# Performance work log

Measured on AMD Instinct MI355X. Metric: run time of the kernel, lower is better.

The kernel has to match this reference:

```python
import jax, jax.numpy as jnp
import numpy as np

D_MODEL = 2048
N_HEAD = 16
HEAD_DIM = D_MODEL // N_HEAD
FFN_DIM = 4 * D_MODEL
B, T = 2, 2048
EPS = float(np.finfo(np.float32).eps)  # torch nn.RMSNorm default eps


def _rmsnorm(x, w):
    return x * jax.lax.rsqrt(jnp.mean(x * x, axis=-1, keepdims=True) + EPS) * w


def _apply_rope(x, cos, sin):
    # x: (B,H,T,hd); cos/sin: (T,hd) with each frequency repeated twice
    cos_pair = cos[..., 0::2]
    sin_pair = sin[..., 0::2]
    x_even = x[..., 0::2]
    x_odd = x[..., 1::2]
    rot_even = x_even * cos_pair - x_odd * sin_pair
    rot_odd = x_odd * cos_pair + x_even * sin_pair
    # interleave back: (..., hd//2, 2) -> (..., hd)
    return jnp.stack([rot_even, rot_odd], axis=-1).reshape(x.shape)


def setup_inputs() -> dict:
    key = jax.random.key(0)
    ks = jax.random.split(key, 9)
    x = jax.random.normal(ks[0], (B, T, D_MODEL), dtype=jnp.float32)
    # real RoPE cache: freqs repeated twice along last axis (interleaved-pair)
    inv_freq = 1.0 / (10000.0 ** (np.arange(0, HEAD_DIM, 2, dtype=np.float32) / HEAD_DIM))
    ang = np.arange(T, dtype=np.float32)[:, None] * inv_freq[None, :]  # (T, hd/2)
    ang2 = np.repeat(ang, 2, axis=-1)  # (T, hd)
    rope_cache = jnp.stack([jnp.cos(jnp.asarray(ang2)), jnp.sin(jnp.asarray(ang2))], axis=0)
    s = 0.02
    return {
        "x": x,
        "rope_cache": rope_cache,
        "attn_norm_w": jnp.ones((D_MODEL,), jnp.float32),
        "qkv_w": s * jax.random.normal(ks[1], (3 * D_MODEL, D_MODEL), jnp.float32),
        "q_norm_w": jnp.ones((HEAD_DIM,), jnp.float32),
        "k_norm_w": jnp.ones((HEAD_DIM,), jnp.float32),
        "out_proj_w": s * jax.random.normal(ks[2], (D_MODEL, D_MODEL), jnp.float32),
        "mlp_norm_w": jnp.ones((D_MODEL,), jnp.float32),
        "mlp_in_w": s * jax.random.normal(ks[3], (FFN_DIM, D_MODEL), jnp.float32),
        "mlp_out_w": s * jax.random.normal(ks[4], (D_MODEL, FFN_DIM), jnp.float32),
    }


def reference(x, rope_cache, attn_norm_w, qkv_w, q_norm_w, k_norm_w,
              out_proj_w, mlp_norm_w, mlp_in_w, mlp_out_w):
    cos, sin = rope_cache[0], rope_cache[1]
    b, t, d = x.shape
    h = _rmsnorm(x, attn_norm_w)
    qkv = h @ qkv_w.T  # (B,T,3D)
    q, k, v = jnp.split(qkv, 3, axis=-1)
    q = q.reshape(b, t, N_HEAD, HEAD_DIM).transpose(0, 2, 1, 3)
    k = k.reshape(b, t, N_HEAD, HEAD_DIM).transpose(0, 2, 1, 3)
    v = v.reshape(b, t, N_HEAD, HEAD_DIM).transpose(0, 2, 1, 3)
    q = _rmsnorm(_apply_rope(q, cos, sin), q_norm_w)
    k = _rmsnorm(_apply_rope(k, cos, sin), k_norm_w)
    scale = 1.0 / jnp.sqrt(jnp.float32(HEAD_DIM))
    scores = jnp.einsum('bhqd,bhkd->bhqk', q, k) * scale
    causal = jnp.tril(jnp.ones((t, t), dtype=bool))
    scores = jnp.where(causal, scores, -jnp.inf)
    attn = jax.nn.softmax(scores, axis=-1)
    attn_out = jnp.einsum('bhqk,bhkd->bhqd', attn, v)
    attn_out = attn_out.transpose(0, 2, 1, 3).reshape(b, t, d)
    x = x + attn_out @ out_proj_w.T
    m = _rmsnorm(x, mlp_norm_w) @ mlp_in_w.T
    m = jnp.square(jax.nn.relu(m))
    return x + m @ mlp_out_w.T
```

## Files before the change

### kernel.cpp

```cpp
#include <hip/hip_runtime.h>
#include <stdint.h>

#define TT 2048
#define DM 2048
#define NH 16
#define HD 128
#define FFN 8192
#define MR 4096
#define EPSF 1.1920928955078125e-07f
#define NEGBIG (-1.0e30f)

typedef __attribute__((ext_vector_type(8))) short short8;
typedef __attribute__((ext_vector_type(4))) float f32x4;
typedef unsigned short u16;
typedef unsigned int u32;

__device__ __forceinline__ float bf2f(u32 u) {
    return __uint_as_float((u & 0xffffu) << 16);
}
__device__ __forceinline__ u16 f2bf(float f) {
    u32 x = __float_as_uint(f);
    return (u16)((x + 0x7fffu + ((x >> 16) & 1u)) >> 16);
}
__device__ __forceinline__ void load8f(const u16* p, float* v) {
    uint4 d = *(const uint4*)p;
    v[0] = bf2f(d.x); v[1] = bf2f(d.x >> 16);
    v[2] = bf2f(d.y); v[3] = bf2f(d.y >> 16);
    v[4] = bf2f(d.z); v[5] = bf2f(d.z >> 16);
    v[6] = bf2f(d.w); v[7] = bf2f(d.w >> 16);
}
__device__ __forceinline__ void load8f32(const float* p, float* v) {
    float4 a = *(const float4*)p, b = *(const float4*)(p + 4);
    v[0]=a.x; v[1]=a.y; v[2]=a.z; v[3]=a.w; v[4]=b.x; v[5]=b.y; v[6]=b.z; v[7]=b.w;
}
__device__ __forceinline__ void store8bf(u16* p, const float* v) {
    uint4 o;
    o.x = (u32)f2bf(v[0]) | ((u32)f2bf(v[1]) << 16);
    o.y = (u32)f2bf(v[2]) | ((u32)f2bf(v[3]) << 16);
    o.z = (u32)f2bf(v[4]) | ((u32)f2bf(v[5]) << 16);
    o.w = (u32)f2bf(v[6]) | ((u32)f2bf(v[7]) << 16);
    *(uint4*)p = o;
}
__device__ __forceinline__ uint4 cvt8_f32_bf16(const float* p) {
    float4 a = *(const float4*)p, b = *(const float4*)(p + 4);
    uint4 o;
    o.x = (u32)f2bf(a.x) | ((u32)f2bf(a.y) << 16);
    o.y = (u32)f2bf(a.z) | ((u32)f2bf(a.w) << 16);
    o.z = (u32)f2bf(b.x) | ((u32)f2bf(b.y) << 16);
    o.w = (u32)f2bf(b.z) | ((u32)f2bf(b.w) << 16);
    return o;
}
__device__ __forceinline__ void gload_lds16(const void* g, void* l) {
    __builtin_amdgcn_global_load_lds((const __attribute__((address_space(1))) u32*)g,
                                     (__attribute__((address_space(3))) u32*)l, 16, 0, 0);
}

__global__ __launch_bounds__(256)
void cvt_w(const float* __restrict__ S, u16* __restrict__ D) {
    size_t i = ((size_t)blockIdx.x * 256 + threadIdx.x) * 8;
    *(uint4*)(D + i) = cvt8_f32_bf16(S + i);
}

__global__ __launch_bounds__(256)
void rmsnorm_k(const float* __restrict__ X, const float* __restrict__ W, u16* __restrict__ O) {
    const int row = blockIdx.x, tid = threadIdx.x;
    float v[8];
    load8f32(X + (size_t)row * DM + tid * 8, v);
    float ssq = 0.f;
#pragma unroll
    for (int i = 0; i < 8; ++i) ssq += v[i] * v[i];
#pragma unroll
    for (int d = 1; d < 64; d <<= 1) ssq += __shfl_xor(ssq, d);
    __shared__ float red[4];
    if ((tid & 63) == 0) red[tid >> 6] = ssq;
    __syncthreads();
    ssq = red[0] + red[1] + red[2] + red[3];
    const float inv = rsqrtf(ssq * (1.f / DM) + EPSF);
    float wv[8], o[8];
    load8f32(W + tid * 8, wv);
#pragma unroll
    for (int i = 0; i < 8; ++i) o[i] = v[i] * inv * wv[i];
    store8bf(O + (size_t)row * DM + tid * 8, o);
}

template<int EPI>
__global__ __launch_bounds__(256)
void gemm_bt(const u16* __restrict__ A, const u16* __restrict__ Bw,
             const float* __restrict__ Res, void* __restrict__ Cp,
             int M, int N, int K, int ldb) {
    __shared__ alignas(16) u16 As[128 * 32];
    __shared__ alignas(16) u16 Bs[128 * 32];
    const int tid = threadIdx.x;
    const int lane = tid & 63, w = tid >> 6;
    const int quad = lane >> 4, col = lane & 15;
    const int n0 = blockIdx.x * 128, m0 = blockIdx.y * 128;
    const int wm = (w >> 1) * 64, wn = (w & 1) * 64;

    const int c0 = tid, c1 = tid + 256;
    const int ar0 = c0 >> 2, aq0 = (c0 & 3) ^ ((ar0 >> 1) & 3);
    const int ar1 = c1 >> 2, aq1 = (c1 & 3) ^ ((ar1 >> 1) & 3);
    const u16* agp0 = A  + (size_t)(m0 + ar0) * K + aq0 * 8;
    const u16* agp1 = A  + (size_t)(m0 + ar1) * K + aq1 * 8;
    const u16* bgp0 = Bw + (size_t)(n0 + ar0) * ldb + aq0 * 8;
    const u16* bgp1 = Bw + (size_t)(n0 + ar1) * ldb + aq1 * 8;
    u16* al0 = As + c0 * 8; u16* al1 = As + c1 * 8;
    u16* bl0 = Bs + c0 * 8; u16* bl1 = Bs + c1 * 8;

    int aoff[4], boff[4];
#pragma unroll
    for (int i = 0; i < 4; ++i) {
        int r = wm + i * 16 + col;
        aoff[i] = r * 32 + (quad ^ ((r >> 1) & 3)) * 8;
        r = wn + i * 16 + col;
        boff[i] = r * 32 + (quad ^ ((r >> 1) & 3)) * 8;
    }

    f32x4 acc[4][4];
#pragma unroll
    for (int i = 0; i < 4; ++i)
#pragma unroll
        for (int j = 0; j < 4; ++j) acc[i][j] = (f32x4){0.f, 0.f, 0.f, 0.f};

    for (int kt = 0; kt < K; kt += 32) {
        __syncthreads();
        gload_lds16(agp0 + kt, al0);
        gload_lds16(agp1 + kt, al1);
        gload_lds16(bgp0 + kt, bl0);
        gload_lds16(bgp1 + kt, bl1);
        __syncthreads();
        short8 af[4], bfr[4];
#pragma unroll
        for (int i = 0; i < 4; ++i) af[i] = *(const short8*)(As + aoff[i]);
#pragma unroll
        for (int i = 0; i < 4; ++i) bfr[i] = *(const short8*)(Bs + boff[i]);
#pragma unroll
        for (int mi = 0; mi < 4; ++mi)
#pragma unroll
            for (int ni = 0; ni < 4; ++ni)
                acc[mi][ni] = __builtin_amdgcn_mfma_f32_16x16x32_bf16(af[mi], bfr[ni], acc[mi][ni], 0, 0, 0);
    }

#pragma unroll
    for (int mi = 0; mi < 4; ++mi)
#pragma unroll
        for (int ni = 0; ni < 4; ++ni) {
            const int rbase = m0 + wm + mi * 16 + quad * 4;
            const int cc = n0 + wn + ni * 16 + col;
#pragma unroll
            for (int rr = 0; rr < 4; ++rr) {
                float v = acc[mi][ni][rr];
                size_t idx = (size_t)(rbase + rr) * N + cc;
                if (EPI == 0) ((u16*)Cp)[idx] = f2bf(v);
                else if (EPI == 1) { float t = fmaxf(v, 0.f); ((u16*)Cp)[idx] = f2bf(t * t); }
                else ((float*)Cp)[idx] = v + Res[idx];
            }
        }
}

__global__ __launch_bounds__(256)
void rope_split_k(const u16* __restrict__ QKV, const float* __restrict__ RC,
                  const float* __restrict__ QW, const float* __restrict__ KW,
                  u16* __restrict__ Qo, u16* __restrict__ Ko, u16* __restrict__ Vo) {
    const int row = blockIdx.x;
    const int t = row & (TT - 1), b = row >> 11;
    const int tid = threadIdx.x, h = tid >> 4, j = tid & 15;
    const size_t qb = (size_t)row * (3 * DM) + h * HD + j * 8;
    float q[8], k[8], cs[8], sn[8];
    load8f(QKV + qb, q);
    load8f(QKV + qb + DM, k);
    uint4 vv = *(const uint4*)(QKV + qb + 2 * DM);
    load8f32(RC + (size_t)t * HD + j * 8, cs);
    load8f32(RC + (size_t)(TT + t) * HD + j * 8, sn);
    float qr[8], kr[8];
#pragma unroll
    for (int p = 0; p < 4; ++p) {
        float c = cs[2 * p], s = sn[2 * p];
        qr[2*p]   = q[2*p]   * c - q[2*p+1] * s;
        qr[2*p+1] = q[2*p+1] * c + q[2*p]   * s;
        kr[2*p]   = k[2*p]   * c - k[2*p+1] * s;
        kr[2*p+1] = k[2*p+1] * c + k[2*p]   * s;
    }
    float sq = 0.f, sk = 0.f;
#pragma unroll
    for (int i = 0; i < 8; ++i) { sq += qr[i] * qr[i]; sk += kr[i] * kr[i]; }
#pragma unroll
    for (int d = 1; d < 16; d <<= 1) { sq += __shfl_xor(sq, d); sk += __shfl_xor(sk, d); }
    const float iq = rsqrtf(sq * (1.f / HD) + EPSF);
    const float ik = rsqrtf(sk * (1.f / HD) + EPSF);
    float qw[8], kw[8], oq[8], ok[8];
    load8f32(QW + j * 8, qw); load8f32(KW + j * 8, kw);
#pragma unroll
    for (int i = 0; i < 8; ++i) { oq[i] = qr[i] * iq * qw[i]; ok[i] = kr[i] * ik * kw[i]; }
    const size_t ob = ((size_t)(b * NH + h) * TT + t) * HD + j * 8;
    store8bf(Qo + ob, oq);
    store8bf(Ko + ob, ok);
    *(uint4*)(Vo + ob) = vv;
}

__global__ __launch_bounds__(256)
void transpose_v(const u16* __restrict__ V, u16* __restrict__ Vt) {
    __shared__ alignas(16) u16 tile[64][72];
    const int bh = blockIdx.z;
    const int t0 = blockIdx.x * 64, d0 = blockIdx.y * 64;
    const int tid = threadIdx.x;
#pragma unroll
    for (int i = 0; i < 2; ++i) {
        int c = i * 256 + tid;
        int r = c >> 3, cc = (c & 7) * 8;
        *(uint4*)(&tile[r][cc]) = *(const uint4*)(V + ((size_t)bh * TT + t0 + r) * HD + d0 + cc);
    }
    __syncthreads();
#pragma unroll
    for (int i = 0; i < 2; ++i) {
        int c = i * 256 + tid;
        int dc = c >> 3, rr = (c & 7) * 8;
        u16 tmp[8];
#pragma unroll
        for (int kk = 0; kk < 8; ++kk) tmp[kk] = tile[rr + kk][dc];
        uint4 o;
        o.x = (u32)tmp[0] | ((u32)tmp[1] << 16);
        o.y = (u32)tmp[2] | ((u32)tmp[3] << 16);
        o.z = (u32)tmp[4] | ((u32)tmp[5] << 16);
        o.w = (u32)tmp[6] | ((u32)tmp[7] << 16);
        *(uint4*)(Vt + ((size_t)bh * HD + d0 + dc) * TT + t0 + rr) = o;
    }
}

__global__ __launch_bounds__(256)
void attn_k(const u16* __restrict__ Q, const u16* __restrict__ Kg,
            const u16* __restrict__ Vt, u16* __restrict__ O) {
    __shared__ alignas(16) u16 k_lds[2][64 * 128];
    __shared__ alignas(16) u16 v_lds[2][128 * 64];
    __shared__ alignas(16) u16 p_lds[4 * 16 * 72];
    const int qt = gridDim.x - 1 - blockIdx.x;
    const int bh = blockIdx.y;
    const int tid = threadIdx.x, lane = tid & 63, w = tid >> 6;
    const int quad = lane >> 4, col = lane & 15;
    const int qbase = qt * 64;
    const int qrow = qbase + w * 16 + col;

    short8 qf[4];
    const u16* qp = Q + ((size_t)bh * TT + qrow) * HD;
#pragma unroll
    for (int s = 0; s < 4; ++s) qf[s] = *(const short8*)(qp + s * 32 + quad * 8);

    const u16* kp[4]; const u16* vp[4];
#pragma unroll
    for (int i = 0; i < 4; ++i) {
        int lin = i * 256 + tid;
        int r = lin >> 4, sl = lin & 15;
        int gq = sl ^ (r & 15);
        kp[i] = Kg + ((size_t)bh * TT + r) * HD + gq * 8;
    }
#pragma unroll
    for (int i = 0; i < 4; ++i) {
        int lin = i * 256 + tid;
        int r = lin >> 3, sl = lin & 7;
        int gq = sl ^ (r & 7);
        vp[i] = Vt + ((size_t)bh * HD + r) * TT + gq * 8;
    }

    f32x4 oacc[8];
#pragma unroll
    for (int i = 0; i < 8; ++i) oacc[i] = (f32x4){0.f, 0.f, 0.f, 0.f};
    float mrow[4] = {NEGBIG, NEGBIG, NEGBIG, NEGBIG};
    float lrow[4] = {0.f, 0.f, 0.f, 0.f};
    const float scale = 0.08838834764831845f;

    u16* kcur = k_lds[0]; u16* knxt = k_lds[1];
    u16* vcur = v_lds[0]; u16* vnxt = v_lds[1];
#pragma unroll
    for (int i = 0; i < 4; ++i) gload_lds16(kp[i], kcur + (i * 256 + tid) * 8);
#pragma unroll
    for (int i = 0; i < 4; ++i) gload_lds16(vp[i], vcur + (i * 256 + tid) * 8);

    for (int kt = 0; kt <= qt; ++kt) {
        const int kb = kt * 64;
        __syncthreads();

        if (kt < qt) {
            const int kb2 = kb + 64;
#pragma unroll
            for (int i = 0; i < 4; ++i) gload_lds16(kp[i] + (size_t)kb2 * HD, knxt + (i * 256 + tid) * 8);
#pragma unroll
            for (int i = 0; i < 4; ++i) gload_lds16(vp[i] + kb2, vnxt + (i * 256 + tid) * 8);
        }

        f32x4 sfr[4];
#pragma unroll
        for (int ni = 0; ni < 4; ++ni) sfr[ni] = (f32x4){0.f, 0.f, 0.f, 0.f};
        __builtin_amdgcn_s_setprio(1);
#pragma unroll
        for (int ni = 0; ni < 4; ++ni) {
            const int r = ni * 16 + col;
#pragma unroll
            for (int s = 0; s < 4; ++s) {
                int sl = (s * 4 + quad) ^ (r & 15);
                short8 kf = *(const short8*)(kcur + r * 128 + sl * 8);
                sfr[ni] = __builtin_amdgcn_mfma_f32_16x16x32_bf16(qf[s], kf, sfr[ni], 0, 0, 0);
            }
        }
        __builtin_amdgcn_s_setprio(0);
        const bool diag = (kt == qt);
#pragma unroll
        for (int ni = 0; ni < 4; ++ni) {
            const int key = kb + ni * 16 + col;
#pragma unroll
            for (int rr = 0; rr < 4; ++rr) {
                float v = sfr[ni][rr] * scale;
                int qv = qbase + w * 16 + quad * 4 + rr;
                if (diag && key > qv) v = NEGBIG;
                sfr[ni][rr] = v;
            }
        }
        float mx[4];
#pragma unroll
        for (int rr = 0; rr < 4; ++rr)
            mx[rr] = fmaxf(fmaxf(sfr[0][rr], sfr[1][rr]), fmaxf(sfr[2][rr], sfr[3][rr]));
#pragma unroll
        for (int d = 1; d < 16; d <<= 1)
#pragma unroll
            for (int rr = 0; rr < 4; ++rr) mx[rr] = fmaxf(mx[rr], __shfl_xor(mx[rr], d));
        if (__any((mx[0] > mrow[0]) || (mx[1] > mrow[1]) ||
                  (mx[2] > mrow[2]) || (mx[3] > mrow[3]))) {
#pragma unroll
            for (int rr = 0; rr < 4; ++rr) {
                float mn = fmaxf(mrow[rr], mx[rr]);
                float a = __expf(mrow[rr] - mn);
                mrow[rr] = mn;
                lrow[rr] *= a;
#pragma unroll
                for (int i = 0; i < 8; ++i) oacc[i][rr] *= a;
            }
        }
        float rs[4] = {0.f, 0.f, 0.f, 0.f};
#pragma unroll
        for (int ni = 0; ni < 4; ++ni)
#pragma unroll
            for (int rr = 0; rr < 4; ++rr) {
                float p = __expf(sfr[ni][rr] - mrow[rr]);
                sfr[ni][rr] = p;
                rs[rr] += p;
            }
#pragma unroll
        for (int d = 1; d < 16; d <<= 1)
#pragma unroll
            for (int rr = 0; rr < 4; ++rr) rs[rr] += __shfl_xor(rs[rr], d);
#pragma unroll
        for (int rr = 0; rr < 4; ++rr) lrow[rr] += rs[rr];
#pragma unroll
        for (int ni = 0; ni < 4; ++ni)
#pragma unroll
            for (int rr = 0; rr < 4; ++rr)
                p_lds[(w * 16 + quad * 4 + rr) * 72 + ni * 16 + col] = f2bf(sfr[ni][rr]);
        __builtin_amdgcn_s_setprio(1);
#pragma unroll
        for (int ks = 0; ks < 2; ++ks) {
            short8 pa = *(const short8*)(p_lds + (w * 16 + col) * 72 + ks * 32 + quad * 8);
#pragma unroll
            for (int di = 0; di < 8; ++di) {
                int r = di * 16 + col;
                int sl = (ks * 4 + quad) ^ (r & 7);
                short8 vb = *(const short8*)(vcur + r * 64 + sl * 8);
                oacc[di] = __builtin_amdgcn_mfma_f32_16x16x32_bf16(pa, vb, oacc[di], 0, 0, 0);
            }
        }
        __builtin_amdgcn_s_setprio(0);
        { u16* t = kcur; kcur = knxt; knxt = t; }
        { u16* t = vcur; vcur = vnxt; vnxt = t; }
    }
    const int b = bh >> 4, h = bh & 15;
#pragma unroll
    for (int di = 0; di < 8; ++di)
#pragma unroll
        for (int rr = 0; rr < 4; ++rr) {
            int trow = qbase + w * 16 + quad * 4 + rr;
            float ov = oacc[di][rr] / lrow[rr];
            O[((size_t)(b * TT + trow)) * DM + h * HD + di * 16 + col] = f2bf(ov);
        }
}

extern "C" void kernel_launch(void* const* d_in, const int* in_sizes, int n_in,
                              void* d_out, int out_size, void* d_ws, size_t ws_size,
                              hipStream_t stream) {
    const float* x    = (const float*)d_in[0];
    const float* rc   = (const float*)d_in[1];
    const float* anw  = (const float*)d_in[2];
    const float* qkvw = (const float*)d_in[3];
    const float* qnw  = (const float*)d_in[4];
    const float* knw  = (const float*)d_in[5];
    const float* opw  = (const float*)d_in[6];
    const float* mnw  = (const float*)d_in[7];
    const float* miw  = (const float*)d_in[8];
    const float* mow  = (const float*)d_in[9];

    char* ws = (char*)d_ws;
    u16* hbuf = (u16*)(ws);
    u16* Wq   = (u16*)(ws + (16ll  << 20));
    u16* Wmi  = (u16*)(ws + (16ll  << 20));
    u16* vt   = (u16*)(ws + (16ll  << 20));
    u16* aout = (u16*)(ws + (32ll  << 20));
    u16* Wmo  = (u16*)(ws + (48ll  << 20));
    u16* qkv  = (u16*)(ws + (48ll  << 20));
    u16* mbuf = (u16*)(ws + (80ll  << 20));
    u16* qh   = (u16*)(ws + (96ll  << 20));
    u16* Wo   = (u16*)(ws + (112ll << 20));
    u16* kh   = (u16*)(ws + (112ll << 20));
    u16* vh   = (u16*)(ws);
    float* xo = (float*)d_out;

    rmsnorm_k<<<MR, 256, 0, stream>>>(x, anw, hbuf);
    cvt_w<<<6144, 256, 0, stream>>>(qkvw, Wq);
    gemm_bt<0><<<dim3(48, 32), 256, 0, stream>>>(hbuf, Wq, nullptr, qkv, MR, 3 * DM, DM, DM);
    rope_split_k<<<MR, 256, 0, stream>>>(qkv, rc, qnw, knw, qh, kh, vh);
    transpose_v<<<dim3(32, 2, 32), 256, 0, stream>>>(vh, vt);
    attn_k<<<dim3(32, 32), 256, 0, stream>>>(qh, kh, vt, aout);
    cvt_w<<<2048, 256, 0, stream>>>(opw, Wo);
    cvt_w<<<8192, 256, 0, stream>>>(mow, Wmo);
    gemm_bt<2><<<dim3(16, 32), 256, 0, stream>>>(aout, Wo, x, xo, MR, DM, DM, DM);
    rmsnorm_k<<<MR, 256, 0, stream>>>(xo, mnw, hbuf);
    cvt_w<<<8192, 256, 0, stream>>>(miw, Wmi);
    gemm_bt<1><<<dim3(32, 32), 256, 0, stream>>>(hbuf, Wmi, nullptr, mbuf, MR, FFN / 2, DM, DM);
    gemm_bt<2><<<dim3(16, 32), 256, 0, stream>>>(mbuf, Wmo, xo, xo, MR, DM, FFN / 2, FFN);
    gemm_bt<1><<<dim3(32, 32), 256, 0, stream>>>(hbuf, Wmi + (size_t)(FFN / 2) * DM, nullptr, mbuf, MR, FFN / 2, DM, DM);
    gemm_bt<2><<<dim3(16, 32), 256, 0, stream>>>(mbuf, Wmo + FFN / 2, xo, xo, MR, DM, FFN / 2, FFN);
}
```

Before: 1.061 ms.

## Add 256x256-tile 4-stage pipelined GEMM for QKV and MLP-in projections

Introduces a new GEMM kernel with 256x256 output tiles, 512 threads, a 4-deep LDS ring buffer fed by direct global-to-LDS loads, XOR-swizzled LDS layout, and an XCD-aware block index remap. It replaces the smaller-tile GEMM for the QKV projection and both MLP-in halves, aiming to raise arithmetic intensity per loaded byte and hide memory latency. The larger tile uses 128 KB of LDS and many accumulator registers, which limits occupancy and yields fewer blocks (256-384) for the 256 compute units.

```diff
diff --git a/kernel.cpp b/kernel.cpp
--- a/kernel.cpp
+++ b/kernel.cpp
@@ -153,6 +153,105 @@
                 if (EPI == 0) ((u16*)Cp)[idx] = f2bf(v);
                 else if (EPI == 1) { float t = fmaxf(v, 0.f); ((u16*)Cp)[idx] = f2bf(t * t); }
                 else ((float*)Cp)[idx] = v + Res[idx];
+            }
+        }
+}
+
+template<int EPI>
+__global__ __launch_bounds__(512, 2)
+void gemm_big(const u16* __restrict__ A, const u16* __restrict__ Bw,
+              void* __restrict__ Cp, int M, int N, int K, int ldb) {
+    __shared__ alignas(16) u16 As[4][256 * 32];
+    __shared__ alignas(16) u16 Bs[4][256 * 32];
+    const int tid = threadIdx.x;
+    const int lane = tid & 63, w = tid >> 6;
+    const int wr = w >> 2, wc = w & 3;
+    const int quad = lane >> 4, colL = lane & 15;
+
+    const int nbx = N >> 8;
+    const int nwg = gridDim.x;
+    const int cpx = nwg >> 3;
+    const int bid = blockIdx.x;
+    const int swz = (bid & 7) * cpx + (bid >> 3);
+    const int by = swz / nbx, bx = swz - by * nbx;
+    const int m0 = by << 8, n0 = bx << 8;
+
+    const int r0 = tid >> 2,       q0 = (tid & 3) ^ ((r0 >> 1) & 3);
+    const int p1 = tid + 512;
+    const int r1 = p1 >> 2,        q1 = (p1 & 3) ^ ((r1 >> 1) & 3);
+    const u16* agp0 = A  + (size_t)(m0 + r0) * K   + q0 * 8;
+    const u16* agp1 = A  + (size_t)(m0 + r1) * K   + q1 * 8;
+    const u16* bgp0 = Bw + (size_t)(n0 + r0) * ldb + q0 * 8;
+    const u16* bgp1 = Bw + (size_t)(n0 + r1) * ldb + q1 * 8;
+    const int l0 = tid * 8, l1 = p1 * 8;
+
+    int aoff[8], boff[4];
+#pragma unroll
+    for (int mi = 0; mi < 8; ++mi) {
+        int r = wr * 128 + mi * 16 + colL;
+        aoff[mi] = r * 32 + (quad ^ ((r >> 1) & 3)) * 8;
+    }
+#pragma unroll
+    for (int ni = 0; ni < 4; ++ni) {
+        int r = wc * 64 + ni * 16 + colL;
+        boff[ni] = r * 32 + (quad ^ ((r >> 1) & 3)) * 8;
+    }
+
+    f32x4 acc[8][4];
+#pragma unroll
+    for (int i = 0; i < 8; ++i)
+#pragma unroll
+        for (int j = 0; j < 4; ++j) acc[i][j] = (f32x4){0.f, 0.f, 0.f, 0.f};
+
+    const int KT = K >> 5;
+
+#define GB_STAGE(s) { const int _b = (s) & 3; const size_t _ko = (size_t)(s) * 32; \
+    gload_lds16(agp0 + _ko, &As[_b][l0]); \
+    gload_lds16(agp1 + _ko, &As[_b][l1]); \
+    gload_lds16(bgp0 + _ko, &Bs[_b][l0]); \
+    gload_lds16(bgp1 + _ko, &Bs[_b][l1]); }
+
+    GB_STAGE(0);
+    GB_STAGE(1);
+    GB_STAGE(2);
+
+    for (int t = 0; t < KT; ++t) {
+        const int rem = KT - 1 - t;
+        if (rem >= 2)      asm volatile("s_waitcnt vmcnt(8)" ::: "memory");
+        else if (rem == 1) asm volatile("s_waitcnt vmcnt(4)" ::: "memory");
+        else               asm volatile("s_waitcnt vmcnt(0)" ::: "memory");
+        __builtin_amdgcn_s_barrier();
+        if (t + 3 < KT) GB_STAGE(t + 3);
+        const u16* ab = As[t & 3];
+        const u16* bb = Bs[t & 3];
+        short8 af[8], bfr[4];
+#pragma unroll
+        for (int mi = 0; mi < 8; ++mi) af[mi] = *(const short8*)(ab + aoff[mi]);
+#pragma unroll
+        for (int ni = 0; ni < 4; ++ni) bfr[ni] = *(const short8*)(bb + boff[ni]);
+        __builtin_amdgcn_s_setprio(1);
+#pragma unroll
+        for (int mi = 0; mi < 8; ++mi)
+#pragma unroll
+            for (int ni = 0; ni < 4; ++ni)
+                acc[mi][ni] = __builtin_amdgcn_mfma_f32_16x16x32_bf16(af[mi], bfr[ni], acc[mi][ni], 0, 0, 0);
+        __builtin_amdgcn_s_setprio(0);
+        __builtin_amdgcn_sched_barrier(0);
+    }
+#undef GB_STAGE
+
+#pragma unroll
+    for (int mi = 0; mi < 8; ++mi)
+#pragma unroll
+        for (int ni = 0; ni < 4; ++ni) {
+            const int rbase = m0 + wr * 128 + mi * 16 + quad * 4;
+            const int cc = n0 + wc * 64 + ni * 16 + colL;
+#pragma unroll
+            for (int rr = 0; rr < 4; ++rr) {
+                float v = acc[mi][ni][rr];
+                size_t idx = (size_t)(rbase + rr) * N + cc;
+                if (EPI == 0) ((u16*)Cp)[idx] = f2bf(v);
+                else { float tq = fmaxf(v, 0.f); ((u16*)Cp)[idx] = f2bf(tq * tq); }
             }
         }
 }
@@ -411,7 +510,7 @@
 
     rmsnorm_k<<<MR, 256, 0, stream>>>(x, anw, hbuf);
     cvt_w<<<6144, 256, 0, stream>>>(qkvw, Wq);
-    gemm_bt<0><<<dim3(48, 32), 256, 0, stream>>>(hbuf, Wq, nullptr, qkv, MR, 3 * DM, DM, DM);
+    gemm_big<0><<<384, 512, 0, stream>>>(hbuf, Wq, qkv, MR, 3 * DM, DM, DM);
     rope_split_k<<<MR, 256, 0, stream>>>(qkv, rc, qnw, knw, qh, kh, vh);
     transpose_v<<<dim3(32, 2, 32), 256, 0, stream>>>(vh, vt);
     attn_k<<<dim3(32, 32), 256, 0, stream>>>(qh, kh, vt, aout);
@@ -420,8 +519,8 @@
     gemm_bt<2><<<dim3(16, 32), 256, 0, stream>>>(aout, Wo, x, xo, MR, DM, DM, DM);
     rmsnorm_k<<<MR, 256, 0, stream>>>(xo, mnw, hbuf);
     cvt_w<<<8192, 256, 0, stream>>>(miw, Wmi);
-    gemm_bt<1><<<dim3(32, 32), 256, 0, stream>>>(hbuf, Wmi, nullptr, mbuf, MR, FFN / 2, DM, DM);
+    gemm_big<1><<<256, 512, 0, stream>>>(hbuf, Wmi, mbuf, MR, FFN / 2, DM, DM);
     gemm_bt<2><<<dim3(16, 32), 256, 0, stream>>>(mbuf, Wmo, xo, xo, MR, DM, FFN / 2, FFN);
-    gemm_bt<1><<<dim3(32, 32), 256, 0, stream>>>(hbuf, Wmi + (size_t)(FFN / 2) * DM, nullptr, mbuf, MR, FFN / 2, DM, DM);
+    gemm_big<1><<<256, 512, 0, stream>>>(hbuf, Wmi + (size_t)(FFN / 2) * DM, mbuf, MR, FFN / 2, DM, DM);
     gemm_bt<2><<<dim3(16, 32), 256, 0, stream>>>(mbuf, Wmo + FFN / 2, xo, xo, MR, DM, FFN / 2, FFN);
 }
```

After: 1.047 ms. No clear change (-1.3%).
